# Kernel tuning notes

Measured on AMD Instinct MI355X. Metric: run time of the kernel, lower is better.

## Reference

```python
import jax, jax.numpy as jnp
import numpy as np

MAX_DF = 0.05
MAX_DPHI = 0.5
MAX_DA = 0.5
MIN_LENGTH = 2
N_BASE = 9
NEG = -jnp.inf


def _wrap(x):
    return (x + jnp.pi) % (2 * jnp.pi) - jnp.pi


def _link_single(tok):
    """tok: (W, K, 9) -> (new_tok9 (W,K,9), member (W,K) int32 local chain id or -1, count int32)."""
    W, K, _ = tok.shape
    snr = tok[..., 0]
    f_s, f_e = tok[..., 3], tok[..., 4]
    A_s, A_e = tok[..., 5], tok[..., 6]
    ps, pe = tok[..., 7], tok[..., 8]

    # ---- edge compatibility mask E[w, kp, kn] for w in 0..W-2 ----
    fe = f_e[:-1, :, None]; fs = f_s[1:, None, :]
    fm = (fe + fs) * 0.5
    f_ok = ~((fm > 0) & (jnp.abs(fe - fs) / jnp.where(fm > 0, fm, 1.0) > MAX_DF))
    p_ok = jnp.abs(_wrap(ps[1:, None, :] - pe[:-1, :, None])) <= MAX_DPHI
    ae = A_e[:-1, :, None]; an = A_s[1:, None, :]
    am = jnp.maximum(ae, an)
    a_ok = ~((am > 0) & (jnp.abs(ae - an) / jnp.where(am > 0, am, 1.0) > MAX_DA))
    E = (snr[:-1, :, None] > 0) & (snr[1:, None, :] > 0) & f_ok & p_ok & a_ok

    # ---- DP over windows: best-SNR chain ending at (w,k), seeded ONLY at window 0
    # (the torch code adds singletons for w>=1 AFTER the DP, so they never extend) ----
    best0 = jnp.where(snr[0] > 0, snr[0], NEG)

    def dp_step(best_prev, inp):
        Ew, snr_next = inp
        cand = jnp.where(Ew, best_prev[:, None] + snr_next[None, :], NEG)
        best_edge = cand.max(axis=0)
        arg = cand.argmax(axis=0).astype(jnp.int32)  # first max == smallest kp (torch tie rule)
        has = best_edge > NEG
        best_new = jnp.where(has, best_edge, NEG)
        return best_new, (best_new, jnp.where(has, arg, -1))

    _, (best_rest, pred_rest) = jax.lax.scan(dp_step, best0, (E, snr[1:]))
    best_dp = jnp.concatenate([best0[None], best_rest], 0)        # (W,K)
    pred = jnp.concatenate([jnp.full((1, K), -1, jnp.int32), pred_rest], 0)

    reach = best_dp > NEG
    # positive-snr tokens unreachable from window 0 become length-1 singleton chains
    score = jnp.where(reach, best_dp, jnp.where(snr > 0, snr, NEG))
    valid = score > NEG

    # ---- chain lengths ----
    def len_step(Lprev, inp):
        pw, vw = inp
        L = jnp.where(pw >= 0, Lprev[jnp.clip(pw, 0, K - 1)] + 1,
                      jnp.where(vw, 1, 0))
        return L, L

    L0 = jnp.where(valid[0], 1, 0).astype(jnp.int32)
    _, Lr = jax.lax.scan(len_step, L0, (pred[1:], valid[1:]))
    L = jnp.concatenate([L0[None], Lr], 0)                        # (W,K) int32

    # ---- backtrack token path for every endpoint: bpath[e, s] = token at window w_e - s ----
    def backtrack(w, k):
        def step(carry, _):
            cw, ck = carry
            nk = jnp.where((ck >= 0) & (cw > 0),
                           pred[jnp.clip(cw, 0, W - 1), jnp.clip(ck, 0, K - 1)], -1)
            return (cw - 1, nk), ck
        _, bp = jax.lax.scan(step, (w, k), None, length=W)
        return bp

    Wg, Kg = jnp.meshgrid(jnp.arange(W, dtype=jnp.int32),
                          jnp.arange(K, dtype=jnp.int32), indexing='ij')
    bpath = jax.vmap(backtrack)(Wg.reshape(-1), Kg.reshape(-1))   # (W*K, W) int32

    # ---- greedy non-overlapping assignment by descending total SNR ----
    order = jnp.argsort(-score.reshape(-1))  # stable; -inf endpoints sort last
    s_arr = jnp.arange(W)
    flatL = L.reshape(-1)
    flatV = valid.reshape(-1)

    def greedy_step(carry, e):
        used, counter = carry
        we = e // K
        Le = flatL[e]
        bp = bpath[e]
        act = s_arr < Le
        rows = jnp.where(act, we - s_arr, W)          # OOB rows dropped
        cols = jnp.clip(bp, 0, K - 1)
        M = jnp.zeros((W, K), bool).at[rows, cols].set(act, mode='drop')
        take = flatV[e] & ~jnp.any(M & used)
        used = used | (M & take)
        enrich = take & (Le >= MIN_LENGTH)
        cid = jnp.where(enrich, counter, -1)
        counter = counter + enrich.astype(jnp.int32)
        return (used, counter), (enrich, cid)

    (_, count), (enrich_o, cid_o) = jax.lax.scan(
        greedy_step, (jnp.zeros((W, K), bool), jnp.int32(0)), order)
    enrich = jnp.zeros((W * K,), bool).at[order].set(enrich_o)
    cid = jnp.full((W * K,), -1, jnp.int32).at[order].set(cid_o)

    # ---- per-slot membership + within-chain successor token (slots are disjoint) ----
    act = enrich[:, None] & (s_arr[None, :] < flatL[:, None])     # (W*K, W)
    we_all = (jnp.arange(W * K, dtype=jnp.int32) // K)[:, None]
    rows = jnp.where(act, we_all - s_arr[None, :], W)
    cols = jnp.clip(bpath, 0, K - 1)
    member = jnp.full((W, K), -1, jnp.int32).at[rows, cols].set(
        jnp.broadcast_to(cid[:, None], act.shape), mode='drop')
    succ_vals = jnp.concatenate(
        [jnp.full((W * K, 1), -1, jnp.int32), bpath[:, :-1].astype(jnp.int32)], 1)
    succ = jnp.full((W, K), -1, jnp.int32).at[rows, cols].set(succ_vals, mode='drop')

    # ---- enrichment 1: combined SNR = sqrt(sum snr^2) over each chain ----
    is_mem = member >= 0
    seg = jnp.where(is_mem, member, W * K)            # dummy segment for non-members
    snr2 = jnp.where(is_mem, snr * snr, 0.0)
    chain_snr2 = jax.ops.segment_sum(snr2.reshape(-1), seg.reshape(-1),
                                     num_segments=W * K + 1)
    safe = jnp.where(chain_snr2 > 0, chain_snr2, 1.0)
    snr_new = jnp.where(is_mem, jnp.sqrt(safe)[seg], snr)

    # ---- enrichment 2: boundary smoothing. Each boundary touches disjoint fields,
    # so all boundaries of all chains are independent and fully vectorizable. ----
    has_succ = succ >= 0
    nk = jnp.clip(succ, 0, K - 1)

    def nxt(col):  # value of col at (w+1, succ[w,k])
        shifted = jnp.concatenate([col[1:], jnp.zeros((1, K), col.dtype)], 0)
        return jnp.take_along_axis(shifted, nk, axis=1)

    f_avg = (f_e + nxt(f_s)) * 0.5
    A_avg = (A_e + nxt(A_s)) * 0.5
    ps_n = nxt(ps)
    corr = _wrap(ps_n - pe)
    f_e_new = jnp.where(has_succ, f_avg, f_e)
    A_e_new = jnp.where(has_succ, A_avg, A_e)
    pe_new = jnp.where(has_succ, pe + corr * 0.5, pe)
    rows2 = jnp.where(has_succ, jnp.arange(W)[:, None] + 1, W)
    f_s_new = f_s.at[rows2, nk].set(jnp.where(has_succ, f_avg, 0.0), mode='drop')
    A_s_new = A_s.at[rows2, nk].set(jnp.where(has_succ, A_avg, 0.0), mode='drop')
    ps_new = ps.at[rows2, nk].set(jnp.where(has_succ, ps_n - corr * 0.5, 0.0), mode='drop')

    out9 = jnp.stack([snr_new, tok[..., 1], tok[..., 2], f_s_new, f_e_new,
                      A_s_new, A_e_new, ps_new, pe_new], axis=-1)
    return out9, member, count


def setup_inputs() -> dict:
    key = jax.random.key(0)
    B, W, K, C = 16, 128, 32, 9
    tokens = jax.random.normal(key, (B, W, K, C), dtype=jnp.float32)
    return {"tokens": tokens}


def reference(tokens):
    new9, member, counts = jax.vmap(_link_single)(tokens[..., :N_BASE])
    # chain_counter carries across batch elements
    offsets = jnp.concatenate(
        [jnp.zeros((1,), counts.dtype), jnp.cumsum(counts)[:-1]])
    cid = jnp.where(member >= 0, member + offsets[:, None, None], -1)
    return jnp.concatenate([new9, cid[..., None].astype(tokens.dtype)], -1)
```

## Files before the change

kernel.cpp:

```cpp
#include <hip/hip_runtime.h>
#include <stdint.h>

#define WW 128
#define KK 32
#define NC 9
#define NCELL (WW * KK)
#define SLICES 16

__device__ __forceinline__ float wrapf(float x) {
  const float kPi = 3.14159265358979323846f;
  const float kTwoPi = 6.28318530717958647692f;
  float y = fmodf(x + kPi, kTwoPi);
  y = (y < 0.0f) ? (y + kTwoPi) : y;
  return y - kPi;
}

__device__ __forceinline__ uint32_t ordf(float f) {
  uint32_t u = __float_as_uint(f);
  return (u & 0x80000000u) ? ~u : (u | 0x80000000u);
}

__device__ __forceinline__ uint32_t hs_key(int j) {
  return 0x5EED0C0Du ^ ((uint32_t)j * 0x9E3779B9u);
}

struct Row {
  float snr, fs, fe, As, Ae, ps, pe;
};

__device__ __forceinline__ Row loadRow(const float* __restrict__ T, int w,
                                       int k) {
  const float* C = T + (size_t)(w * KK + k) * NC;
  Row r;
  r.snr = C[0];
  r.fs = C[3];
  r.fe = C[4];
  r.As = C[5];
  r.Ae = C[6];
  r.ps = C[7];
  r.pe = C[8];
  return r;
}

__global__ __launch_bounds__(256) void fused_kernel(
    const float* __restrict__ tokens, float* __restrict__ out,
    uint32_t* __restrict__ ws_u) {
  const int bb = blockIdx.x >> 4;
  const int sl = blockIdx.x & (SLICES - 1);
  const int tid = threadIdx.x;
  const int B = gridDim.x >> 4;
  uint32_t* flags = ws_u;
  uint32_t* flags2 = ws_u + 64;
  uint32_t* chsum = ws_u + 256;
  int* packed = (int*)(ws_u + 4096);
  const float* T = tokens + (size_t)bb * NCELL * NC;

  __shared__ int8_t s_pred[NCELL];
  __shared__ int8_t s_member[NCELL];
  __shared__ int8_t s_succ[NCELL];
  __shared__ int8_t s_chaincol[KK * WW];
  __shared__ int8_t s_predcol[NCELL];
  __shared__ int s_chainlen[KK];
  __shared__ unsigned long long s_win[KK];
  __shared__ int s_count;
  __shared__ int s_wlim;
  __shared__ int s_cnt[64];
  __shared__ int s_mywl;

  const int i = (sl << 8) + tid;
  const int wcell = i >> 5;
  float t0, t1, t2, t3, t4, t5, t6, t7, t8;
  if (sl != 0) {
    const float* C = T + (size_t)i * NC;
    t0 = C[0]; t1 = C[1]; t2 = C[2]; t3 = C[3]; t4 = C[4];
    t5 = C[5]; t6 = C[6]; t7 = C[7]; t8 = C[8];
  }

  if (sl == 0) {
    {
      int* mi = (int*)s_member;
      int* si = (int*)s_succ;
      int* pi = (int*)s_predcol;
      for (int j = tid; j < NCELL / 4; j += 256) {
        mi[j] = -1;
        si[j] = -1;
        pi[j] = -1;
      }
      if (tid < KK) s_win[tid] = 0ull;
    }
    __syncthreads();

    if (tid < 64) {
      const int k = tid & 31;
      const int h = tid >> 5;
      float snr0 = T[k * NC + 0];
      bool v0 = snr0 > 0.0f;
      float prev_best = v0 ? snr0 : -INFINITY;
      int prev_root = k;
      float prev_fe = T[k * NC + 4];
      float prev_Ae = T[k * NC + 6];
      float prev_pe = T[k * NC + 8];
      if (h == 0) {
        s_pred[k] = -1;
        if (v0) {
          unsigned long long key =
              ((unsigned long long)ordf(snr0) << 32) | (uint32_t)(~(uint32_t)k);
          atomicMax(&s_win[k], key);
        }
      }
      Row cur = loadRow(T, 1, k);
      Row nxt = loadRow(T, 2, k);
      for (int w = 1; w < WW; ++w) {
        unsigned long long full = __ballot(prev_best > -INFINITY);
        if (full == 0ull) break;

        int wf = (w + 2 < WW) ? (w + 2) : (WW - 1);
        Row fut = loadRow(T, wf, k);

        bool scur = cur.snr > 0.0f;
        float bestE = -INFINITY;
        int arg = 0;
        unsigned int rem = (unsigned int)full;
        while (rem) {
          int kp0 = __ffs(rem) - 1;
          rem &= rem - 1;
          bool have2 = rem != 0u;
          int kp1 = have2 ? (__ffs(rem) - 1) : kp0;
          if (have2) rem &= rem - 1;
          int kp = h ? kp1 : kp0;
          bool lane_ok = h ? have2 : true;
          float bp = __shfl(prev_best, kp);
          float fe = __shfl(prev_fe, kp);
          float ae = __shfl(prev_Ae, kp);
          float pe = __shfl(prev_pe, kp);
          float fm = (fe + cur.fs) * 0.5f;
          float fden = (fm > 0.0f) ? fm : 1.0f;
          bool fbad = (fm > 0.0f) && (fabsf(fe - cur.fs) / fden > 0.05f);
          float am = fmaxf(ae, cur.As);
          float aden = (am > 0.0f) ? am : 1.0f;
          bool abad = (am > 0.0f) && (fabsf(ae - cur.As) / aden > 0.5f);
          bool pok = fabsf(wrapf(cur.ps - pe)) <= 0.5f;
          if (lane_ok && scur && !fbad && !abad && pok) {
            float cand = bp + cur.snr;
            if (cand > bestE) { bestE = cand; arg = kp; }
          }
        }
        float ob = __shfl_xor(bestE, 32);
        int oa = __shfl_xor(arg, 32);
        float b0 = h ? ob : bestE;
        float b1 = h ? bestE : ob;
        int a0 = h ? oa : arg;
        int a1 = h ? arg : oa;
        bool take0 = (b0 > b1) || ((b0 == b1) && (a0 <= a1));
        float bE = take0 ? b0 : b1;
        int aC = take0 ? a0 : a1;
        bool has = bE > -INFINITY;
        if (h == 0) s_pred[w * KK + k] = (int8_t)(has ? aC : -1);
        int rsrc = has ? aC : 0;
        int rootc = __shfl(prev_root, rsrc);
        int root_new = has ? rootc : k;
        float bnew = has ? bE : -INFINITY;
        if (has && h == 0) {
          int idx = w * KK + k;
          unsigned long long key = ((unsigned long long)ordf(bnew) << 32) |
                                   (uint32_t)(~(uint32_t)idx);
          atomicMax(&s_win[root_new], key);
        }
        prev_best = bnew;
        prev_root = root_new;
        prev_fe = cur.fe;
        prev_Ae = cur.Ae;
        prev_pe = cur.pe;
        cur = nxt;
        nxt = fut;
      }
    }
    __syncthreads();

    if (tid < KK) {
      unsigned long long wk = s_win[tid];
      bool exists = (wk != 0ull);
      int idx = exists ? (int)(~(uint32_t)(wk & 0xFFFFFFFFull)) : -1;
      int we = idx >> 5;
      int ke = idx & 31;
      bool enr = exists && (we >= 1);
      int cid = 0;
      for (int r2 = 0; r2 < KK; ++r2) {
        unsigned long long k2 = __shfl(wk, r2);
        int e2 = __shfl((int)enr, r2);
        if (e2 && k2 > wk) cid++;
      }
      unsigned long long bal = __ballot(enr);
      int total = __popcll(bal);
      int wml = enr ? we : -1;
      for (int d = 1; d < KK; d <<= 1) {
        int o = __shfl_xor(wml, d);
        wml = (o > wml) ? o : wml;
      }
      if (tid == 0) {
        s_count = total;
        s_wlim = wml;
      }
      if (enr) {
        s_chainlen[cid] = we + 1;
        int cw = we, ck = ke, prevc = -1;
        while (cw >= 0) {
          int cell = (cw << 5) | ck;
          s_member[cell] = (int8_t)cid;
          s_succ[cell] = (int8_t)prevc;
          if (prevc >= 0) s_predcol[((cw + 1) << 5) | prevc] = (int8_t)ck;
          s_chaincol[cid * WW + cw] = (int8_t)ck;
          prevc = ck;
          ck = s_pred[cell];
          cw--;
        }
      }
    }
    __syncthreads();

    if (tid < KK && tid < s_count) {
      int len = s_chainlen[tid];
      float sum = 0.0f;
      for (int w = 0; w < len; ++w) {
        int col = s_chaincol[tid * WW + w];
        float s = T[(size_t)(w * KK + col) * NC + 0];
        sum += s * s;
      }
      __hip_atomic_store(&chsum[bb * KK + tid], __float_as_uint(sum),
                         __ATOMIC_RELAXED, __HIP_MEMORY_SCOPE_AGENT);
    }
    __syncthreads();

    {
      int nlim = (s_wlim + 1) * KK;
      for (int j = tid; j < nlim; j += 256) {
        int pk = (s_member[j] & 0xFF) | ((s_succ[j] & 0xFF) << 8) |
                 ((s_predcol[j] & 0xFF) << 16);
        __hip_atomic_store(&packed[bb * NCELL + j], pk, __ATOMIC_RELAXED,
                           __HIP_MEMORY_SCOPE_AGENT);
      }
    }
    __syncthreads();
    if (tid == 0) {
      __threadfence();
      uint32_t v = (uint32_t)s_count | ((uint32_t)(s_wlim + 1) << 8);
      __hip_atomic_store(&flags2[bb], v ^ hs_key(bb), __ATOMIC_RELEASE,
                         __HIP_MEMORY_SCOPE_AGENT);
      __hip_atomic_store(&flags[bb], v, __ATOMIC_RELEASE,
                         __HIP_MEMORY_SCOPE_AGENT);
    }
  }

  if (tid < B) {
    uint32_t v, c2;
    for (;;) {
      v = __hip_atomic_load(&flags[tid], __ATOMIC_ACQUIRE,
                            __HIP_MEMORY_SCOPE_AGENT);
      c2 = __hip_atomic_load(&flags2[tid], __ATOMIC_ACQUIRE,
                             __HIP_MEMORY_SCOPE_AGENT);
      if (((v & 0xFFu) <= 32u) && ((v >> 8) <= 128u) &&
          (c2 == (v ^ hs_key(tid))))
        break;
      __builtin_amdgcn_s_sleep(2);
    }
    s_cnt[tid] = (int)(v & 0xFFu);
    if (tid == bb) s_mywl = (int)(v >> 8) - 1;
  }
  __syncthreads();
  int off = 0;
  for (int j = 0; j < bb; ++j) off += s_cnt[j];
  const int wlim = s_mywl;

  if (sl == 0) {
    const float* C = T + (size_t)i * NC;
    t0 = C[0]; t1 = C[1]; t2 = C[2]; t3 = C[3]; t4 = C[4];
    t5 = C[5]; t6 = C[6]; t7 = C[7]; t8 = C[8];
  }
  int mm = -1, sc = -1, pc = -1;
  if (wcell <= wlim) {
    int pk = __hip_atomic_load(&packed[bb * NCELL + i], __ATOMIC_RELAXED,
                               __HIP_MEMORY_SCOPE_AGENT);
    mm = (int)(int8_t)(pk & 0xFF);
    sc = (int)(int8_t)((pk >> 8) & 0xFF);
    pc = (int)(int8_t)((pk >> 16) & 0xFF);
  }
  float o0 = t0;
  if (mm >= 0) {
    uint32_t cs = __hip_atomic_load(&chsum[bb * KK + mm], __ATOMIC_RELAXED,
                                    __HIP_MEMORY_SCOPE_AGENT);
    o0 = sqrtf(__uint_as_float(cs));
  }
  float o3 = t3, o5 = t5, o7 = t7;
  if (pc >= 0) {
    const float* P = T + (size_t)((wcell - 1) * KK + pc) * NC;
    float fep = P[4], aep = P[6], pep = P[8];
    o3 = (fep + t3) * 0.5f;
    o5 = (aep + t5) * 0.5f;
    float corr = wrapf(t7 - pep);
    o7 = t7 - corr * 0.5f;
  }
  float o4 = t4, o6 = t6, o8 = t8;
  if (sc >= 0) {
    const float* S = T + (size_t)((wcell + 1) * KK + sc) * NC;
    float fsn = S[3], asn = S[5], psn = S[7];
    o4 = (t4 + fsn) * 0.5f;
    o6 = (t6 + asn) * 0.5f;
    float corr = wrapf(psn - t8);
    o8 = t8 + corr * 0.5f;
  }
  float* O = out + ((size_t)bb * NCELL + i) * 10;
  O[0] = o0; O[1] = t1; O[2] = t2; O[3] = o3; O[4] = o4;
  O[5] = o5; O[6] = o6; O[7] = o7; O[8] = o8;
  O[9] = (mm >= 0) ? (float)(mm + off) : -1.0f;
}

extern "C" void kernel_launch(void* const* d_in, const int* in_sizes, int n_in,
                              void* d_out, int out_size, void* d_ws,
                              size_t ws_size, hipStream_t stream) {
  const float* tokens = (const float*)d_in[0];
  float* out = (float*)d_out;
  int B = in_sizes[0] / (WW * KK * NC);
  uint32_t* ws_u = (uint32_t*)d_ws;
  fused_kernel<<<dim3(B * SLICES), dim3(256), 0, stream>>>(tokens, out, ws_u);
}
```

Measured before the change: 28.21 us.

## Precompute edge masks in chunks by helper warps, overlapped with the serial DP

```diff
diff --git a/kernel.cpp b/kernel.cpp
--- a/kernel.cpp
+++ b/kernel.cpp
@@ -6,6 +6,8 @@
 #define NC 9
 #define NCELL (WW * KK)
 #define SLICES 16
+#define CH 16
+#define NCHUNK 8
 
 __device__ __forceinline__ float wrapf(float x) {
   const float kPi = 3.14159265358979323846f;
@@ -24,22 +26,38 @@
   return 0x5EED0C0Du ^ ((uint32_t)j * 0x9E3779B9u);
 }
 
-struct Row {
-  float snr, fs, fe, As, Ae, ps, pe;
-};
-
-__device__ __forceinline__ Row loadRow(const float* __restrict__ T, int w,
-                                       int k) {
-  const float* C = T + (size_t)(w * KK + k) * NC;
-  Row r;
-  r.snr = C[0];
-  r.fs = C[3];
-  r.fe = C[4];
-  r.As = C[5];
-  r.Ae = C[6];
-  r.ps = C[7];
-  r.pe = C[8];
-  return r;
+__device__ __forceinline__ void compute_chunk(const float* __restrict__ T,
+                                              int base, int nw,
+                                              uint32_t* __restrict__ mbuf,
+                                              float* __restrict__ sbuf, int t0,
+                                              int stride) {
+  for (int p = t0; p < nw * KK; p += stride) {
+    int w = base + (p >> 5);
+    int k = p & 31;
+    const float* C = T + (size_t)(w * KK + k) * NC;
+    float snr = C[0];
+    uint32_t mask = 0u;
+    if (snr > 0.0f) {
+      float fs = C[3], As = C[5], ps = C[7];
+      const float* Pr = T + (size_t)((w - 1) * KK) * NC;
+#pragma unroll 4
+      for (int kp = 0; kp < KK; ++kp) {
+        float fe = Pr[kp * NC + 4];
+        float ae = Pr[kp * NC + 6];
+        float pe = Pr[kp * NC + 8];
+        float fm = (fe + fs) * 0.5f;
+        float fden = (fm > 0.0f) ? fm : 1.0f;
+        bool fbad = (fm > 0.0f) && (fabsf(fe - fs) / fden > 0.05f);
+        float am = fmaxf(ae, As);
+        float aden = (am > 0.0f) ? am : 1.0f;
+        bool abad = (am > 0.0f) && (fabsf(ae - As) / aden > 0.5f);
+        bool pok = fabsf(wrapf(ps - pe)) <= 0.5f;
+        if (!fbad && !abad && pok) mask |= (1u << kp);
+      }
+    }
+    mbuf[p] = mask;
+    sbuf[p] = snr;
+  }
 }
 
 __global__ __launch_bounds__(256) void fused_kernel(
@@ -58,12 +76,15 @@
   __shared__ int8_t s_pred[NCELL];
   __shared__ int8_t s_member[NCELL];
   __shared__ int8_t s_succ[NCELL];
+  __shared__ int8_t s_predcol[NCELL];
   __shared__ int8_t s_chaincol[KK * WW];
-  __shared__ int8_t s_predcol[NCELL];
   __shared__ int s_chainlen[KK];
   __shared__ unsigned long long s_win[KK];
+  __shared__ uint32_t s_mask[2][CH * KK];
+  __shared__ float s_snr[2][CH * KK];
   __shared__ int s_count;
   __shared__ int s_wlim;
+  __shared__ int s_alive;
   __shared__ int s_cnt[64];
   __shared__ int s_mywl;
 
@@ -87,95 +108,77 @@
         pi[j] = -1;
       }
       if (tid < KK) s_win[tid] = 0ull;
-    }
+      if (tid == 0) s_alive = 1;
+    }
+    compute_chunk(T, 1, CH - 1, s_mask[0], s_snr[0], tid, 256);
     __syncthreads();
 
-    if (tid < 64) {
-      const int k = tid & 31;
-      const int h = tid >> 5;
+    float prev_best = -INFINITY;
+    int prev_root = 0;
+    if (tid < KK) {
+      const int k = tid;
       float snr0 = T[k * NC + 0];
       bool v0 = snr0 > 0.0f;
-      float prev_best = v0 ? snr0 : -INFINITY;
-      int prev_root = k;
-      float prev_fe = T[k * NC + 4];
-      float prev_Ae = T[k * NC + 6];
-      float prev_pe = T[k * NC + 8];
-      if (h == 0) {
-        s_pred[k] = -1;
-        if (v0) {
-          unsigned long long key =
-              ((unsigned long long)ordf(snr0) << 32) | (uint32_t)(~(uint32_t)k);
-          atomicMax(&s_win[k], key);
+      prev_best = v0 ? snr0 : -INFINITY;
+      prev_root = k;
+      s_pred[k] = -1;
+      if (v0) {
+        unsigned long long key =
+            ((unsigned long long)ordf(snr0) << 32) | (uint32_t)(~(uint32_t)k);
+        atomicMax(&s_win[k], key);
+      }
+    }
+
+    for (int c = 0; c < NCHUNK; ++c) {
+      if (tid < KK) {
+        const int k = tid;
+        const int base = (c == 0) ? 1 : CH * c;
+        const int nw = (c == 0) ? CH - 1 : CH;
+        const uint32_t* mk = s_mask[c & 1];
+        const float* sn = s_snr[c & 1];
+        for (int j = 0; j < nw; ++j) {
+          uint32_t live = (uint32_t)__ballot(prev_best > -INFINITY);
+          if (live == 0u) {
+            if (tid == 0) s_alive = 0;
+            break;
+          }
+          int w = base + j;
+          uint32_t mask = mk[(j << 5) + k] & live;
+          float snr_c = sn[(j << 5) + k];
+          float bestE = -INFINITY;
+          int arg = 0;
+          int rsel = k;
+          uint32_t rem = live;
+          while (rem) {
+            int r = __ffs(rem) - 1;
+            rem &= rem - 1;
+            float bp = __shfl(prev_best, r);
+            int rt = __shfl(prev_root, r);
+            float cand = bp + snr_c;
+            if (((mask >> r) & 1u) && cand > bestE) {
+              bestE = cand;
+              arg = r;
+              rsel = rt;
+            }
+          }
+          bool has = bestE > -INFINITY;
+          s_pred[(w << 5) + k] = (int8_t)(has ? arg : -1);
+          if (has) {
+            int idx = (w << 5) + k;
+            unsigned long long key = ((unsigned long long)ordf(bestE) << 32) |
+                                     (uint32_t)(~(uint32_t)idx);
+            atomicMax(&s_win[rsel], key);
+          }
+          prev_best = has ? bestE : -INFINITY;
+          prev_root = has ? rsel : k;
         }
-      }
-      Row cur = loadRow(T, 1, k);
-      Row nxt = loadRow(T, 2, k);
-      for (int w = 1; w < WW; ++w) {
-        unsigned long long full = __ballot(prev_best > -INFINITY);
-        if (full == 0ull) break;
-
-        int wf = (w + 2 < WW) ? (w + 2) : (WW - 1);
-        Row fut = loadRow(T, wf, k);
-
-        bool scur = cur.snr > 0.0f;
-        float bestE = -INFINITY;
-        int arg = 0;
-        unsigned int rem = (unsigned int)full;
-        while (rem) {
-          int kp0 = __ffs(rem) - 1;
-          rem &= rem - 1;
-          bool have2 = rem != 0u;
-          int kp1 = have2 ? (__ffs(rem) - 1) : kp0;
-          if (have2) rem &= rem - 1;
-          int kp = h ? kp1 : kp0;
-          bool lane_ok = h ? have2 : true;
-          float bp = __shfl(prev_best, kp);
-          float fe = __shfl(prev_fe, kp);
-          float ae = __shfl(prev_Ae, kp);
-          float pe = __shfl(prev_pe, kp);
-          float fm = (fe + cur.fs) * 0.5f;
-          float fden = (fm > 0.0f) ? fm : 1.0f;
-          bool fbad = (fm > 0.0f) && (fabsf(fe - cur.fs) / fden > 0.05f);
-          float am = fmaxf(ae, cur.As);
-          float aden = (am > 0.0f) ? am : 1.0f;
-          bool abad = (am > 0.0f) && (fabsf(ae - cur.As) / aden > 0.5f);
-          bool pok = fabsf(wrapf(cur.ps - pe)) <= 0.5f;
-          if (lane_ok && scur && !fbad && !abad && pok) {
-            float cand = bp + cur.snr;
-            if (cand > bestE) { bestE = cand; arg = kp; }
-          }
-        }
-        float ob = __shfl_xor(bestE, 32);
-        int oa = __shfl_xor(arg, 32);
-        float b0 = h ? ob : bestE;
-        float b1 = h ? bestE : ob;
-        int a0 = h ? oa : arg;
-        int a1 = h ? arg : oa;
-        bool take0 = (b0 > b1) || ((b0 == b1) && (a0 <= a1));
-        float bE = take0 ? b0 : b1;
-        int aC = take0 ? a0 : a1;
-        bool has = bE > -INFINITY;
-        if (h == 0) s_pred[w * KK + k] = (int8_t)(has ? aC : -1);
-        int rsrc = has ? aC : 0;
-        int rootc = __shfl(prev_root, rsrc);
-        int root_new = has ? rootc : k;
-        float bnew = has ? bE : -INFINITY;
-        if (has && h == 0) {
-          int idx = w * KK + k;
-          unsigned long long key = ((unsigned long long)ordf(bnew) << 32) |
-                                   (uint32_t)(~(uint32_t)idx);
-          atomicMax(&s_win[root_new], key);
-        }
-        prev_best = bnew;
-        prev_root = root_new;
-        prev_fe = cur.fe;
-        prev_Ae = cur.Ae;
-        prev_pe = cur.pe;
-        cur = nxt;
-        nxt = fut;
-      }
-    }
-    __syncthreads();
+      } else if (tid >= 64 && c + 1 < NCHUNK) {
+        compute_chunk(T, CH * (c + 1), CH, s_mask[(c + 1) & 1],
+                      s_snr[(c + 1) & 1], tid - 64, 192);
+      }
+      __syncthreads();
+      if (!s_alive) break;
+    }
 
     if (tid < KK) {
       unsigned long long wk = s_win[tid];
```

After: 62.62 us. 2.22x slower.

## Stage DP token rows in LDS with double-buffered chunk prefetch

Applied to the files above, without the earlier changes.

```diff
diff --git a/kernel.cpp b/kernel.cpp
--- a/kernel.cpp
+++ b/kernel.cpp
@@ -6,6 +6,8 @@
 #define NC 9
 #define NCELL (WW * KK)
 #define SLICES 16
+#define CH 16
+#define NCHUNK 8
 
 __device__ __forceinline__ float wrapf(float x) {
   const float kPi = 3.14159265358979323846f;
@@ -24,21 +26,33 @@
   return 0x5EED0C0Du ^ ((uint32_t)j * 0x9E3779B9u);
 }
 
-struct Row {
+__device__ __forceinline__ bool gate_ok(float fe, float ae, float pe, float fs,
+                                        float As, float ps) {
+  float fm = (fe + fs) * 0.5f;
+  float fden = (fm > 0.0f) ? fm : 1.0f;
+  bool fbad = (fm > 0.0f) && (fabsf(fe - fs) / fden > 0.05f);
+  float am = fmaxf(ae, As);
+  float aden = (am > 0.0f) ? am : 1.0f;
+  bool abad = (am > 0.0f) && (fabsf(ae - As) / aden > 0.5f);
+  bool pok = fabsf(wrapf(ps - pe)) <= 0.5f;
+  return !fbad && !abad && pok;
+}
+
+struct LRow {
   float snr, fs, fe, As, Ae, ps, pe;
 };
 
-__device__ __forceinline__ Row loadRow(const float* __restrict__ T, int w,
-                                       int k) {
-  const float* C = T + (size_t)(w * KK + k) * NC;
-  Row r;
-  r.snr = C[0];
-  r.fs = C[3];
-  r.fe = C[4];
-  r.As = C[5];
-  r.Ae = C[6];
-  r.ps = C[7];
-  r.pe = C[8];
+__device__ __forceinline__ LRow ldRow(const float* __restrict__ rows, int j,
+                                      int k) {
+  const float* R = rows + (j * KK + k) * NC;
+  LRow r;
+  r.snr = R[0];
+  r.fs = R[3];
+  r.fe = R[4];
+  r.As = R[5];
+  r.Ae = R[6];
+  r.ps = R[7];
+  r.pe = R[8];
   return r;
 }
 
@@ -48,7 +62,6 @@
   const int bb = blockIdx.x >> 4;
   const int sl = blockIdx.x & (SLICES - 1);
   const int tid = threadIdx.x;
-  const int B = gridDim.x >> 4;
   uint32_t* flags = ws_u;
   uint32_t* flags2 = ws_u + 64;
   uint32_t* chsum = ws_u + 256;
@@ -58,12 +71,15 @@
   __shared__ int8_t s_pred[NCELL];
   __shared__ int8_t s_member[NCELL];
   __shared__ int8_t s_succ[NCELL];
+  __shared__ int8_t s_predcol[NCELL];
   __shared__ int8_t s_chaincol[KK * WW];
-  __shared__ int8_t s_predcol[NCELL];
   __shared__ int s_chainlen[KK];
+  __shared__ float s_chainsum[KK];
   __shared__ unsigned long long s_win[KK];
+  __shared__ __align__(16) float s_rows[2][CH * KK * NC];
   __shared__ int s_count;
   __shared__ int s_wlim;
+  __shared__ int s_alive;
   __shared__ int s_cnt[64];
   __shared__ int s_mywl;
 
@@ -87,20 +103,27 @@
         pi[j] = -1;
       }
       if (tid < KK) s_win[tid] = 0ull;
+      if (tid == 0) s_alive = 1;
+    }
+    {
+      const float4* s4 = (const float4*)(T + 1 * KK * NC);
+      float4* d4 = (float4*)s_rows[0];
+      for (int j = tid; j < (CH - 1) * KK * NC / 4; j += 256) d4[j] = s4[j];
     }
     __syncthreads();
 
+    float prev_best = -INFINITY, prev_fe = 0.f, prev_Ae = 0.f, prev_pe = 0.f;
+    int prev_root = 0;
     if (tid < 64) {
       const int k = tid & 31;
-      const int h = tid >> 5;
       float snr0 = T[k * NC + 0];
       bool v0 = snr0 > 0.0f;
-      float prev_best = v0 ? snr0 : -INFINITY;
-      int prev_root = k;
-      float prev_fe = T[k * NC + 4];
-      float prev_Ae = T[k * NC + 6];
-      float prev_pe = T[k * NC + 8];
-      if (h == 0) {
+      prev_best = v0 ? snr0 : -INFINITY;
+      prev_root = k;
+      prev_fe = T[k * NC + 4];
+      prev_Ae = T[k * NC + 6];
+      prev_pe = T[k * NC + 8];
+      if ((tid >> 5) == 0) {
         s_pred[k] = -1;
         if (v0) {
           unsigned long long key =
@@ -108,74 +131,93 @@
           atomicMax(&s_win[k], key);
         }
       }
-      Row cur = loadRow(T, 1, k);
-      Row nxt = loadRow(T, 2, k);
-      for (int w = 1; w < WW; ++w) {
-        unsigned long long full = __ballot(prev_best > -INFINITY);
-        if (full == 0ull) break;
-
-        int wf = (w + 2 < WW) ? (w + 2) : (WW - 1);
-        Row fut = loadRow(T, wf, k);
-
-        bool scur = cur.snr > 0.0f;
-        float bestE = -INFINITY;
-        int arg = 0;
-        unsigned int rem = (unsigned int)full;
-        while (rem) {
-          int kp0 = __ffs(rem) - 1;
-          rem &= rem - 1;
-          bool have2 = rem != 0u;
-          int kp1 = have2 ? (__ffs(rem) - 1) : kp0;
-          if (have2) rem &= rem - 1;
-          int kp = h ? kp1 : kp0;
-          bool lane_ok = h ? have2 : true;
-          float bp = __shfl(prev_best, kp);
-          float fe = __shfl(prev_fe, kp);
-          float ae = __shfl(prev_Ae, kp);
-          float pe = __shfl(prev_pe, kp);
-          float fm = (fe + cur.fs) * 0.5f;
-          float fden = (fm > 0.0f) ? fm : 1.0f;
-          bool fbad = (fm > 0.0f) && (fabsf(fe - cur.fs) / fden > 0.05f);
-          float am = fmaxf(ae, cur.As);
-          float aden = (am > 0.0f) ? am : 1.0f;
-          bool abad = (am > 0.0f) && (fabsf(ae - cur.As) / aden > 0.5f);
-          bool pok = fabsf(wrapf(cur.ps - pe)) <= 0.5f;
-          if (lane_ok && scur && !fbad && !abad && pok) {
-            float cand = bp + cur.snr;
-            if (cand > bestE) { bestE = cand; arg = kp; }
+    }
+
+    for (int c = 0; c < NCHUNK; ++c) {
+      if (tid < 64) {
+        const int k = tid & 31;
+        const int h = tid >> 5;
+        const float* rows = s_rows[c & 1];
+        const int wb = (c == 0) ? 1 : CH * c;
+        const int nw = (c == 0) ? CH - 1 : CH;
+        LRow lr = ldRow(rows, 0, k);
+        for (int j = 0; j < nw; ++j) {
+          unsigned long long fullb = __ballot(prev_best > -INFINITY);
+          uint32_t live = (uint32_t)fullb;
+          if (live == 0u) {
+            if (tid == 0) s_alive = 0;
+            break;
           }
+          LRow ln = ldRow(rows, (j + 1 < nw) ? (j + 1) : j, k);
+          const int w = wb + j;
+          bool scur = lr.snr > 0.0f;
+          float bestE = -INFINITY;
+          int arg = 0;
+          if (__popc(live) == 1) {
+            int r = __ffs(live) - 1;
+            float bp = __shfl(prev_best, r);
+            float fe = __shfl(prev_fe, r);
+            float ae = __shfl(prev_Ae, r);
+            float pe = __shfl(prev_pe, r);
+            if (scur && gate_ok(fe, ae, pe, lr.fs, lr.As, lr.ps)) {
+              bestE = bp + lr.snr;
+              arg = r;
+            }
+          } else {
+            uint32_t rem = live;
+            while (rem) {
+              int kp0 = __ffs(rem) - 1;
+              rem &= rem - 1;
+              bool have2 = rem != 0u;
+              int kp1 = have2 ? (__ffs(rem) - 1) : kp0;
+              if (have2) rem &= rem - 1;
+              int kp = h ? kp1 : kp0;
+              bool lane_ok = h ? have2 : true;
+              float bp = __shfl(prev_best, kp);
+              float fe = __shfl(prev_fe, kp);
+              float ae = __shfl(prev_Ae, kp);
+              float pe = __shfl(prev_pe, kp);
+              if (lane_ok && scur &&
+                  gate_ok(fe, ae, pe, lr.fs, lr.As, lr.ps)) {
+                float cand = bp + lr.snr;
+                if (cand > bestE) { bestE = cand; arg = kp; }
+              }
+            }
+            float ob = __shfl_xor(bestE, 32);
+            int oa = __shfl_xor(arg, 32);
+            float b0 = h ? ob : bestE;
+            float b1 = h ? bestE : ob;
+            int a0 = h ? oa : arg;
+            int a1 = h ? arg : oa;
+            bool take0 = (b0 > b1) || ((b0 == b1) && (a0 <= a1));
+            bestE = take0 ? b0 : b1;
+            arg = take0 ? a0 : a1;
+          }
+          bool has = bestE > -INFINITY;
+          if (h == 0) s_pred[(w << 5) + k] = (int8_t)(has ? arg : -1);
+          int rootc = __shfl(prev_root, has ? arg : 0);
+          int root_new = has ? rootc : k;
+          if (has && h == 0) {
+            int idx = (w << 5) + k;
+            unsigned long long key = ((unsigned long long)ordf(bestE) << 32) |
+                                     (uint32_t)(~(uint32_t)idx);
+            atomicMax(&s_win[root_new], key);
+          }
+          prev_best = has ? bestE : -INFINITY;
+          prev_root = root_new;
+          prev_fe = lr.fe;
+          prev_Ae = lr.Ae;
+          prev_pe = lr.pe;
+          lr = ln;
         }
-        float ob = __shfl_xor(bestE, 32);
-        int oa = __shfl_xor(arg, 32);
-        float b0 = h ? ob : bestE;
-        float b1 = h ? bestE : ob;
-        int a0 = h ? oa : arg;
-        int a1 = h ? arg : oa;
-        bool take0 = (b0 > b1) || ((b0 == b1) && (a0 <= a1));
-        float bE = take0 ? b0 : b1;
-        int aC = take0 ? a0 : a1;
-        bool has = bE > -INFINITY;
-        if (h == 0) s_pred[w * KK + k] = (int8_t)(has ? aC : -1);
-        int rsrc = has ? aC : 0;
-        int rootc = __shfl(prev_root, rsrc);
-        int root_new = has ? rootc : k;
-        float bnew = has ? bE : -INFINITY;
-        if (has && h == 0) {
-          int idx = w * KK + k;
-          unsigned long long key = ((unsigned long long)ordf(bnew) << 32) |
-                                   (uint32_t)(~(uint32_t)idx);
-          atomicMax(&s_win[root_new], key);
-        }
-        prev_best = bnew;
-        prev_root = root_new;
-        prev_fe = cur.fe;
-        prev_Ae = cur.Ae;
-        prev_pe = cur.pe;
-        cur = nxt;
-        nxt = fut;
-      }
-    }
-    __syncthreads();
+      } else if (c + 1 < NCHUNK) {
+        const float4* s4 = (const float4*)(T + (size_t)(CH * (c + 1)) * KK * NC);
+        float4* d4 = (float4*)s_rows[(c + 1) & 1];
+        for (int j = tid - 64; j < CH * KK * NC / 4; j += 192) d4[j] = s4[j];
+      }
+      __syncthreads();
+      if (!s_alive) break;
+    }
 
     if (tid < KK) {
       unsigned long long wk = s_win[tid];
@@ -226,6 +268,7 @@
         float s = T[(size_t)(w * KK + col) * NC + 0];
         sum += s * s;
       }
+      s_chainsum[tid] = sum;
       __hip_atomic_store(&chsum[bb * KK + tid], __float_as_uint(sum),
                          __ATOMIC_RELAXED, __HIP_MEMORY_SCOPE_AGENT);
     }
@@ -251,45 +294,54 @@
     }
   }
 
-  if (tid < B) {
-    uint32_t v, c2;
-    for (;;) {
-      v = __hip_atomic_load(&flags[tid], __ATOMIC_ACQUIRE,
-                            __HIP_MEMORY_SCOPE_AGENT);
-      c2 = __hip_atomic_load(&flags2[tid], __ATOMIC_ACQUIRE,
-                             __HIP_MEMORY_SCOPE_AGENT);
-      if (((v & 0xFFu) <= 32u) && ((v >> 8) <= 128u) &&
-          (c2 == (v ^ hs_key(tid))))
-        break;
-      __builtin_amdgcn_s_sleep(2);
-    }
-    s_cnt[tid] = (int)(v & 0xFFu);
-    if (tid == bb) s_mywl = (int)(v >> 8) - 1;
+  {
+    const int need = (sl == 0) ? bb : (bb + 1);
+    if (tid < need) {
+      uint32_t v, c2;
+      for (;;) {
+        v = __hip_atomic_load(&flags[tid], __ATOMIC_ACQUIRE,
+                              __HIP_MEMORY_SCOPE_AGENT);
+        c2 = __hip_atomic_load(&flags2[tid], __ATOMIC_ACQUIRE,
+                               __HIP_MEMORY_SCOPE_AGENT);
+        if (((v & 0xFFu) <= 32u) && ((v >> 8) <= 128u) &&
+            (c2 == (v ^ hs_key(tid))))
+          break;
+        __builtin_amdgcn_s_sleep(2);
+      }
+      if (tid < bb) s_cnt[tid] = (int)(v & 0xFFu);
+      if (tid == bb) s_mywl = (int)(v >> 8) - 1;
+    }
   }
   __syncthreads();
   int off = 0;
   for (int j = 0; j < bb; ++j) off += s_cnt[j];
-  const int wlim = s_mywl;
-
+
+  int mm, sc, pc;
+  float chs = 0.0f;
   if (sl == 0) {
     const float* C = T + (size_t)i * NC;
     t0 = C[0]; t1 = C[1]; t2 = C[2]; t3 = C[3]; t4 = C[4];
     t5 = C[5]; t6 = C[6]; t7 = C[7]; t8 = C[8];
-  }
-  int mm = -1, sc = -1, pc = -1;
-  if (wcell <= wlim) {
-    int pk = __hip_atomic_load(&packed[bb * NCELL + i], __ATOMIC_RELAXED,
-                               __HIP_MEMORY_SCOPE_AGENT);
-    mm = (int)(int8_t)(pk & 0xFF);
-    sc = (int)(int8_t)((pk >> 8) & 0xFF);
-    pc = (int)(int8_t)((pk >> 16) & 0xFF);
-  }
-  float o0 = t0;
-  if (mm >= 0) {
-    uint32_t cs = __hip_atomic_load(&chsum[bb * KK + mm], __ATOMIC_RELAXED,
-                                    __HIP_MEMORY_SCOPE_AGENT);
-    o0 = sqrtf(__uint_as_float(cs));
-  }
+    mm = s_member[i];
+    sc = s_succ[i];
+    pc = s_predcol[i];
+    if (mm >= 0) chs = s_chainsum[mm];
+  } else {
+    mm = -1; sc = -1; pc = -1;
+    if (wcell <= s_mywl) {
+      int pk = __hip_atomic_load(&packed[bb * NCELL + i], __ATOMIC_RELAXED,
+                                 __HIP_MEMORY_SCOPE_AGENT);
+      mm = (int)(int8_t)(pk & 0xFF);
+      sc = (int)(int8_t)((pk >> 8) & 0xFF);
+      pc = (int)(int8_t)((pk >> 16) & 0xFF);
+      if (mm >= 0) {
+        uint32_t cs = __hip_atomic_load(&chsum[bb * KK + mm], __ATOMIC_RELAXED,
+                                        __HIP_MEMORY_SCOPE_AGENT);
+        chs = __uint_as_float(cs);
+      }
+    }
+  }
+  float o0 = (mm >= 0) ? sqrtf(chs) : t0;
   float o3 = t3, o5 = t5, o7 = t7;
   if (pc >= 0) {
     const float* P = T + (size_t)((wcell - 1) * KK + pc) * NC;
```

Result: slower. 29.48 us, median of 2 (+4.5%).
